# Kernel tuning notes

Hardware: AMD Instinct MI355X
Metric: run time of the kernel (lower is better)

The kernel has to match this reference:

```python
import jax, jax.numpy as jnp
import numpy as np

FACTOR = 5  # sampling factor from __init__


def setup_inputs() -> dict:
    key = jax.random.key(0)
    k1, k2, k3, k4 = jax.random.split(key, 4)
    B, L, H, D = 4, 2048, 8, 64
    S = min(FACTOR * int(np.ceil(np.log(L))), L)  # U_part = 40
    return {
        "queries": jax.random.normal(k1, (B, L, H, D), jnp.float32),
        "keys": jax.random.normal(k2, (B, L, H, D), jnp.float32),
        "values": jax.random.normal(k3, (B, L, H, D), jnp.float32),
        "index_sample": jax.random.randint(k4, (L, S), 0, L, jnp.int32),
    }


def reference(queries, keys, values, index_sample):
    B, L_Q, H, D = queries.shape
    L_K = keys.shape[1]
    Q = jnp.transpose(queries, (0, 2, 1, 3))  # [B,H,L_Q,D]
    K = jnp.transpose(keys, (0, 2, 1, 3))     # [B,H,L_K,D]
    V = jnp.transpose(values, (0, 2, 1, 3))   # [B,H,L_K,D]

    u = min(FACTOR * int(np.ceil(np.log(L_Q))), L_Q)  # n_top

    # --- _prob_QK: sampled QK to score queries, then top-u query selection ---
    # K_sample[b,h,q,s,:] = K[b,h,index_sample[q,s],:]  -> [B,H,L_Q,S,D]
    K_sample = K[:, :, index_sample, :]
    Q_K_sample = jnp.einsum('bhqd,bhqsd->bhqs', Q, K_sample)  # [B,H,L_Q,S]
    M = Q_K_sample.max(-1) - Q_K_sample.sum(-1) / L_K         # sparsity measure
    _, M_top = jax.lax.top_k(M, u)                            # [B,H,u] query indices

    Q_reduce = jnp.take_along_axis(Q, M_top[..., None], axis=2)  # [B,H,u,D]
    scale = 1.0 / np.sqrt(D)
    scores = jnp.einsum('bhud,bhkd->bhuk', Q_reduce, K) * scale  # [B,H,u,L_K]

    # --- _update_context causal mask: rows are the FIRST u rows of the full
    # triu(L_Q,L_Q) mask (faithful to original, which does NOT reindex by M_top)
    causal = jnp.triu(jnp.ones((u, L_Q), dtype=bool), 1)
    scores = jnp.where(causal[None, None], -jnp.inf, scores)
    attn = jax.nn.softmax(scores, axis=-1)
    upd = jnp.einsum('bhuk,bhkd->bhud', attn, V)  # [B,H,u,D]

    # --- _get_initial_context (mask_flag=True): running cumsum of V ---
    context = jnp.cumsum(V, axis=2)  # [B,H,L_Q,D]

    # scatter-overwrite selected query positions
    b = jnp.arange(B)[:, None, None]
    h = jnp.arange(H)[None, :, None]
    context = context.at[b, h, M_top].set(upd)

    return jnp.transpose(context, (0, 2, 1, 3))  # [B,L_Q,H,D]
```

## Files before the change

kernel.cpp:

```cpp
#include <hip/hip_runtime.h>
#include <stdint.h>

constexpr int B = 4;
constexpr int L = 2048;
constexpr int H = 8;
constexpr int D = 64;
constexpr int S = 40;
constexpr int U = 40;
constexpr int HD = H * D;
constexpr int NSEG = 8;
constexpr int SEGL = L / NSEG;
constexpr int NC = 64;
constexpr int CL = L / NC;

__device__ __forceinline__ unsigned mono(float v) {
    unsigned u = __float_as_uint(v);
    return (u & 0x80000000u) ? ~u : (u | 0x80000000u);
}

__global__ __launch_bounds__(256) void k_scores(
    const float4* __restrict__ Q4, const float4* __restrict__ K4,
    const int* __restrict__ idxs, float* __restrict__ M)
{
    int i = blockIdx.x;
    int xcd = i & 7;
    int b = xcd >> 1;
    int qc = (i >> 3) * 2 + (xcd & 1);
    int w = threadIdx.x >> 6;
    int lane = threadIdx.x & 63;
    int q = qc * 4 + w;
    int h = lane >> 3;
    int dd = lane & 7;

    const float4* qrow = Q4 + (size_t)(b * L + q) * 128;
    float4 qa = qrow[2 * lane], qb = qrow[2 * lane + 1];

    int v_idx = idxs[q * S + (lane < S ? lane : 0)];

    const float4* kbase = K4 + (size_t)b * L * 128;
    float mx = -INFINITY, sm = 0.f;
    #pragma unroll 8
    for (int s = 0; s < S; ++s) {
        int ki = __shfl(v_idx, s);
        const float4* krow = kbase + (size_t)ki * 128;
        float4 ka = krow[2 * lane], kb = krow[2 * lane + 1];
        float d = qa.x * ka.x + qa.y * ka.y + qa.z * ka.z + qa.w * ka.w
                + qb.x * kb.x + qb.y * kb.y + qb.z * kb.z + qb.w * kb.w;
        d += __shfl_xor(d, 1);
        d += __shfl_xor(d, 2);
        d += __shfl_xor(d, 4);
        mx = fmaxf(mx, d);
        sm += d;
    }
    if (dd == 0)
        M[(b * 8 + h) * L + q] = mx - sm * (1.0f / (float)L);
}

__global__ __launch_bounds__(64) void k_seg_topk(
    const float* __restrict__ M, unsigned long long* __restrict__ cand,
    int* __restrict__ flags)
{
    int blk = blockIdx.x;
    int bh = blk >> 3, seg = blk & 7;
    int lane = threadIdx.x;
    int j0 = seg * SEGL + lane * 4;

    *(int4*)(flags + (size_t)bh * L + j0) = make_int4(0, 0, 0, 0);

    float4 v = *(const float4*)(M + (size_t)bh * L + j0);
    unsigned m[4] = { mono(v.x), mono(v.y), mono(v.z), mono(v.w) };
    int rank[4] = { 0, 0, 0, 0 };

    #pragma unroll 4
    for (int src = 0; src < 64; ++src) {
        #pragma unroll
        for (int slot = 0; slot < 4; ++slot) {
            unsigned bm = __shfl(m[slot], src);
            int bj = src * 4 + slot;
            #pragma unroll
            for (int s = 0; s < 4; ++s) {
                int myj = lane * 4 + s;
                rank[s] += (bm > m[s]) || (bm == m[s] && bj < myj);
            }
        }
    }

    unsigned long long* out = cand + (size_t)blk * U;
    #pragma unroll
    for (int s = 0; s < 4; ++s)
        if (rank[s] < U)
            out[rank[s]] = ((unsigned long long)m[s] << 32)
                         | (unsigned)(~(unsigned)(j0 + s));
}

__global__ __launch_bounds__(256) void k_attn(
    const float4* __restrict__ Q4, const float4* __restrict__ K4,
    const float4* __restrict__ V4, const unsigned long long* __restrict__ cand,
    int* __restrict__ flags, float* __restrict__ upd)
{
    __shared__ unsigned long long cnd[NSEG * U];
    __shared__ int top_idx[U];
    __shared__ __align__(16) float Qs[U * 68];
    __shared__ __align__(16) float Ks[U * 68];
    __shared__ __align__(16) float Vs[U * 68];
    __shared__ float P[U * 41];

    int bh = blockIdx.x;
    int b = bh >> 3, h = bh & 7;
    int tid = threadIdx.x;

    for (int i = tid; i < NSEG * U; i += 256)
        cnd[i] = cand[(size_t)bh * NSEG * U + i];
    __syncthreads();

    {
        unsigned long long ka = cnd[tid < NSEG * U ? tid : 0];
        unsigned long long kb = (tid < NSEG * U - 256) ? cnd[256 + tid] : 0ULL;
        int ra = 0, rb = 0;
        for (int j = 0; j < NSEG * U; ++j) {
            unsigned long long kj = cnd[j];
            ra += (kj > ka);
            rb += (kj > kb);
        }
        if (tid < NSEG * U && ra < U) top_idx[ra] = (int)(~(unsigned)ka);
        if (tid < NSEG * U - 256 && rb < U) top_idx[rb] = (int)(~(unsigned)kb);
    }
    __syncthreads();

    if (tid < U) flags[bh * L + top_idx[tid]] = tid + 1;

    for (int i = tid; i < U * 16; i += 256) {
        int r = i >> 4, d4 = i & 15;
        size_t kvbase = ((size_t)(b * L + r) * H + h) * 16 + d4;
        *(float4*)(Ks + r * 68 + d4 * 4) = K4[kvbase];
        *(float4*)(Vs + r * 68 + d4 * 4) = V4[kvbase];
        *(float4*)(Qs + r * 68 + d4 * 4) =
            Q4[((size_t)(b * L + top_idx[r]) * H + h) * 16 + d4];
    }
    __syncthreads();

    const float scale = 0.125f;
    for (int p = tid; p < U * U; p += 256) {
        int r = p / U, k = p - r * U;
        if (k <= r) {
            float acc = 0.f;
            #pragma unroll
            for (int d = 0; d < D; d += 4) {
                float4 a = *(const float4*)(Qs + r * 68 + d);
                float4 c = *(const float4*)(Ks + k * 68 + d);
                acc += a.x * c.x + a.y * c.y + a.z * c.z + a.w * c.w;
            }
            P[r * 41 + k] = acc * scale;
        }
    }
    __syncthreads();

    if (tid < U) {
        int r = tid;
        float mval = -INFINITY;
        for (int k = 0; k <= r; ++k) mval = fmaxf(mval, P[r * 41 + k]);
        float ssum = 0.f;
        for (int k = 0; k <= r; ++k) {
            float e = expf(P[r * 41 + k] - mval);
            P[r * 41 + k] = e;
            ssum += e;
        }
        float inv = 1.f / ssum;
        for (int k = 0; k <= r; ++k) P[r * 41 + k] *= inv;
    }
    __syncthreads();

    for (int t = tid; t < U * D; t += 256) {
        int r = t >> 6, d = t & 63;
        float acc = 0.f;
        for (int k = 0; k <= r; ++k) acc += P[r * 41 + k] * Vs[k * 68 + d];
        upd[((size_t)bh * U + r) * D + d] = acc;
    }
}

__global__ __launch_bounds__(512) void k_chunksum(
    const float* __restrict__ V, float* __restrict__ partial)
{
    int b = blockIdx.x >> 6;
    int c = blockIdx.x & 63;
    int hd = threadIdx.x;
    const float* vp = V + ((size_t)(b * L + c * CL)) * HD + hd;
    float s = 0.f;
    #pragma unroll
    for (int l = 0; l < CL; ++l) s += vp[(size_t)l * HD];
    partial[((size_t)b * NC + c) * HD + hd] = s;
}

__global__ __launch_bounds__(512) void k_scan(float* __restrict__ partial)
{
    int b = blockIdx.x;
    int hd = threadIdx.x;
    float acc = 0.f;
    #pragma unroll 8
    for (int c = 0; c < NC; ++c) {
        size_t o = ((size_t)b * NC + c) * HD + hd;
        float v = partial[o];
        partial[o] = acc;
        acc += v;
    }
}

__global__ __launch_bounds__(512) void k_cumsum_out(
    const float* __restrict__ V, const float* __restrict__ partial,
    const int* __restrict__ flags, const float* __restrict__ upd,
    float* __restrict__ out)
{
    int b = blockIdx.x >> 6;
    int c = blockIdx.x & 63;
    int hd = threadIdx.x;
    int h = hd >> 6, d = hd & 63;

    float acc = partial[((size_t)b * NC + c) * HD + hd];

    const float* vp = V + ((size_t)(b * L + c * CL)) * HD + hd;
    float*       op = out + ((size_t)(b * L + c * CL)) * HD + hd;
    const int*   fp = flags + (b * H + h) * L + c * CL;
    const float* up = upd + (size_t)(b * H + h) * U * D + d;

    #pragma unroll 4
    for (int l = 0; l < CL; ++l) {
        acc += vp[(size_t)l * HD];
        int f = fp[l];
        op[(size_t)l * HD] = f ? up[(size_t)(f - 1) * D] : acc;
    }
}

extern "C" void kernel_launch(void* const* d_in, const int* in_sizes, int n_in,
                              void* d_out, int out_size, void* d_ws, size_t ws_size,
                              hipStream_t stream)
{
    const float* Q   = (const float*)d_in[0];
    const float* K   = (const float*)d_in[1];
    const float* V   = (const float*)d_in[2];
    const int*  idxs = (const int*)d_in[3];
    float* out = (float*)d_out;

    char* ws = (char*)d_ws;
    float* M       = (float*)(ws);
    int*   flags   = (int*)  (ws + 262144);
    float* upd     = (float*)(ws + 524288);
    float* partial = (float*)(ws + 851968);
    unsigned long long* cand = (unsigned long long*)(ws + 1376256);

    k_scores    <<<B * L / 4,    256, 0, stream>>>((const float4*)Q, (const float4*)K, idxs, M);
    k_seg_topk  <<<B * H * NSEG,  64, 0, stream>>>(M, cand, flags);
    k_attn      <<<B * H,        256, 0, stream>>>((const float4*)Q, (const float4*)K, (const float4*)V,
                                                   cand, flags, upd);
    k_chunksum  <<<B * NC,       512, 0, stream>>>(V, partial);
    k_scan      <<<B,            512, 0, stream>>>(partial);
    k_cumsum_out<<<B * NC,       512, 0, stream>>>(V, partial, flags, upd, out);
}
```

Baseline: 175.8 us.

## Fuse segment top-k into attention kernel and drop separate scan launch

Merges the per-segment top-k kernel into the attention kernel, using 512 threads (8 wavefronts, one per segment) so candidates go straight to shared memory instead of a global buffer. Removes the chunk-prefix scan kernel by having each output block sum the preceding chunk partials itself. Adds nontemporal loads for Q in the scoring kernel and nontemporal stores for the output. Cuts two kernel launches and a global round trip, at the cost of redundant partial summation in the output kernel and fewer blocks doing the top-k work.

```diff
diff --git a/kernel.cpp b/kernel.cpp
--- a/kernel.cpp
+++ b/kernel.cpp
@@ -18,6 +18,13 @@
     return (u & 0x80000000u) ? ~u : (u | 0x80000000u);
 }
 
+typedef float f4v __attribute__((ext_vector_type(4)));
+
+__device__ __forceinline__ float4 ntload4(const float4* p) {
+    f4v v = __builtin_nontemporal_load((const f4v*)p);
+    return make_float4(v.x, v.y, v.z, v.w);
+}
+
 __global__ __launch_bounds__(256) void k_scores(
     const float4* __restrict__ Q4, const float4* __restrict__ K4,
     const int* __restrict__ idxs, float* __restrict__ M)
@@ -33,7 +40,8 @@
     int dd = lane & 7;
 
     const float4* qrow = Q4 + (size_t)(b * L + q) * 128;
-    float4 qa = qrow[2 * lane], qb = qrow[2 * lane + 1];
+    float4 qa = ntload4(qrow + 2 * lane);
+    float4 qb = ntload4(qrow + 2 * lane + 1);
 
     int v_idx = idxs[q * S + (lane < S ? lane : 0)];
 
@@ -56,13 +64,23 @@
         M[(b * 8 + h) * L + q] = mx - sm * (1.0f / (float)L);
 }
 
-__global__ __launch_bounds__(64) void k_seg_topk(
-    const float* __restrict__ M, unsigned long long* __restrict__ cand,
-    int* __restrict__ flags)
-{
-    int blk = blockIdx.x;
-    int bh = blk >> 3, seg = blk & 7;
-    int lane = threadIdx.x;
+__global__ __launch_bounds__(512) void k_topk_attn(
+    const float* __restrict__ M, const float4* __restrict__ Q4,
+    const float4* __restrict__ K4, const float4* __restrict__ V4,
+    int* __restrict__ flags, float* __restrict__ upd)
+{
+    __shared__ unsigned long long cnd[NSEG * U];
+    __shared__ int top_idx[U];
+    __shared__ __align__(16) float Qs[U * 68];
+    __shared__ __align__(16) float Ks[U * 68];
+    __shared__ __align__(16) float Vs[U * 68];
+    __shared__ float P[U * 41];
+
+    int bh = blockIdx.x;
+    int b = bh >> 3, h = bh & 7;
+    int tid = threadIdx.x;
+    int seg = tid >> 6, lane = tid & 63;
+
     int j0 = seg * SEGL + lane * 4;
 
     *(int4*)(flags + (size_t)bh * L + j0) = make_int4(0, 0, 0, 0);
@@ -84,52 +102,24 @@
             }
         }
     }
-
-    unsigned long long* out = cand + (size_t)blk * U;
     #pragma unroll
     for (int s = 0; s < 4; ++s)
         if (rank[s] < U)
-            out[rank[s]] = ((unsigned long long)m[s] << 32)
-                         | (unsigned)(~(unsigned)(j0 + s));
-}
-
-__global__ __launch_bounds__(256) void k_attn(
-    const float4* __restrict__ Q4, const float4* __restrict__ K4,
-    const float4* __restrict__ V4, const unsigned long long* __restrict__ cand,
-    int* __restrict__ flags, float* __restrict__ upd)
-{
-    __shared__ unsigned long long cnd[NSEG * U];
-    __shared__ int top_idx[U];
-    __shared__ __align__(16) float Qs[U * 68];
-    __shared__ __align__(16) float Ks[U * 68];
-    __shared__ __align__(16) float Vs[U * 68];
-    __shared__ float P[U * 41];
-
-    int bh = blockIdx.x;
-    int b = bh >> 3, h = bh & 7;
-    int tid = threadIdx.x;
-
-    for (int i = tid; i < NSEG * U; i += 256)
-        cnd[i] = cand[(size_t)bh * NSEG * U + i];
+            cnd[seg * U + rank[s]] = ((unsigned long long)m[s] << 32)
+                                   | (unsigned)(~(unsigned)(j0 + s));
     __syncthreads();
 
     {
         unsigned long long ka = cnd[tid < NSEG * U ? tid : 0];
-        unsigned long long kb = (tid < NSEG * U - 256) ? cnd[256 + tid] : 0ULL;
-        int ra = 0, rb = 0;
-        for (int j = 0; j < NSEG * U; ++j) {
-            unsigned long long kj = cnd[j];
-            ra += (kj > ka);
-            rb += (kj > kb);
-        }
+        int ra = 0;
+        for (int j = 0; j < NSEG * U; ++j) ra += (cnd[j] > ka);
         if (tid < NSEG * U && ra < U) top_idx[ra] = (int)(~(unsigned)ka);
-        if (tid < NSEG * U - 256 && rb < U) top_idx[rb] = (int)(~(unsigned)kb);
     }
     __syncthreads();
 
     if (tid < U) flags[bh * L + top_idx[tid]] = tid + 1;
 
-    for (int i = tid; i < U * 16; i += 256) {
+    for (int i = tid; i < U * 16; i += 512) {
         int r = i >> 4, d4 = i & 15;
         size_t kvbase = ((size_t)(b * L + r) * H + h) * 16 + d4;
         *(float4*)(Ks + r * 68 + d4 * 4) = K4[kvbase];
@@ -140,7 +130,7 @@
     __syncthreads();
 
     const float scale = 0.125f;
-    for (int p = tid; p < U * U; p += 256) {
+    for (int p = tid; p < U * U; p += 512) {
         int r = p / U, k = p - r * U;
         if (k <= r) {
             float acc = 0.f;
@@ -170,7 +160,7 @@
     }
     __syncthreads();
 
-    for (int t = tid; t < U * D; t += 256) {
+    for (int t = tid; t < U * D; t += 512) {
         int r = t >> 6, d = t & 63;
         float acc = 0.f;
         for (int k = 0; k <= r; ++k) acc += P[r * 41 + k] * Vs[k * 68 + d];
@@ -191,21 +181,7 @@
     partial[((size_t)b * NC + c) * HD + hd] = s;
 }
 
-__global__ __launch_bounds__(512) void k_scan(float* __restrict__ partial)
-{
-    int b = blockIdx.x;
-    int hd = threadIdx.x;
-    float acc = 0.f;
-    #pragma unroll 8
-    for (int c = 0; c < NC; ++c) {
-        size_t o = ((size_t)b * NC + c) * HD + hd;
-        float v = partial[o];
-        partial[o] = acc;
-        acc += v;
-    }
-}
-
-__global__ __launch_bounds__(512) void k_cumsum_out(
+__global__ __launch_bounds__(512) void k_out(
     const float* __restrict__ V, const float* __restrict__ partial,
     const int* __restrict__ flags, const float* __restrict__ upd,
     float* __restrict__ out)
@@ -215,7 +191,9 @@
     int hd = threadIdx.x;
     int h = hd >> 6, d = hd & 63;
 
-    float acc = partial[((size_t)b * NC + c) * HD + hd];
+    float acc = 0.f;
+    const float* pp = partial + (size_t)b * NC * HD + hd;
+    for (int j = 0; j < c; ++j) acc += pp[(size_t)j * HD];
 
     const float* vp = V + ((size_t)(b * L + c * CL)) * HD + hd;
     float*       op = out + ((size_t)(b * L + c * CL)) * HD + hd;
@@ -226,7 +204,8 @@
     for (int l = 0; l < CL; ++l) {
         acc += vp[(size_t)l * HD];
         int f = fp[l];
-        op[(size_t)l * HD] = f ? up[(size_t)(f - 1) * D] : acc;
+        float o = f ? up[(size_t)(f - 1) * D] : acc;
+        __builtin_nontemporal_store(o, op + (size_t)l * HD);
     }
 }
 
@@ -241,17 +220,14 @@
     float* out = (float*)d_out;
 
     char* ws = (char*)d_ws;
-    float* M       = (float*)(ws);
-    int*   flags   = (int*)  (ws + 262144);
-    float* upd     = (float*)(ws + 524288);
-    float* partial = (float*)(ws + 851968);
-    unsigned long long* cand = (unsigned long long*)(ws + 1376256);
-
-    k_scores    <<<B * L / 4,    256, 0, stream>>>((const float4*)Q, (const float4*)K, idxs, M);
-    k_seg_topk  <<<B * H * NSEG,  64, 0, stream>>>(M, cand, flags);
-    k_attn      <<<B * H,        256, 0, stream>>>((const float4*)Q, (const float4*)K, (const float4*)V,
-                                                   cand, flags, upd);
-    k_chunksum  <<<B * NC,       512, 0, stream>>>(V, partial);
-    k_scan      <<<B,            512, 0, stream>>>(partial);
-    k_cumsum_out<<<B * NC,       512, 0, stream>>>(V, partial, flags, upd, out);
-}
+    float* M        = (float*)(ws);
+    int*   flags    = (int*)  (ws + 262144);
+    float* upd      = (float*)(ws + 524288);
+    float* partial  = (float*)(ws + 851968);
+
+    k_scores    <<<B * L / 4, 256, 0, stream>>>((const float4*)Q, (const float4*)K, idxs, M);
+    k_topk_attn <<<B * H,     512, 0, stream>>>(M, (const float4*)Q, (const float4*)K,
+                                                (const float4*)V, flags, upd);
+    k_chunksum  <<<B * NC,    512, 0, stream>>>(V, partial);
+    k_out       <<<B * NC,    512, 0, stream>>>(V, partial, flags, upd, out);
+}
```

New measurement: 189.8 us. 7.9% more time.
